# Optimization experiments

Hardware: AMD Instinct MI355X
Metric: run time of the kernel (lower is better)

The kernel has to match this reference:

```python
import jax, jax.numpy as jnp
import numpy as np

N_EMBD = 1024
N_HEAD = 16
STRIDE = 128
C = 8
SEQ = 2048
BATCH = 2


def _sparse_causal_mask(nd, ns, stride, c, dtype):
    # Faithful vectorization of _sparse_attention_mask:
    # column j is globally visible if (j % stride) >= stride - c (the last c
    # columns of each stride block), each query also sees its own stride block,
    # and everything is causally masked (j <= q).
    j = jnp.arange(ns)
    q = jnp.arange(ns)[:, None]
    col_sel = (j % stride) >= (stride - c)          # strided summary columns
    same_block = (j[None, :] // stride) == (q // stride)  # local block
    causal = j[None, :] <= q
    mask = ((col_sel[None, :] | same_block) & causal).astype(dtype)
    return mask[ns - nd:]


def setup_inputs() -> dict:
    key = jax.random.key(0)
    k1, k2, k3 = jax.random.split(key, 3)
    inputs = jax.random.normal(k1, (BATCH, SEQ, N_EMBD), dtype=jnp.float32)
    w_attn = jax.random.normal(k2, (N_EMBD, 3 * N_EMBD), dtype=jnp.float32) * 0.02
    b_attn = jnp.zeros((3 * N_EMBD,), dtype=jnp.float32)
    proj_std = 0.02 / np.sqrt(2 * 24)  # n_layer = 24
    w_proj = jax.random.normal(k3, (N_EMBD, N_EMBD), dtype=jnp.float32) * proj_std
    b_proj = jnp.zeros((N_EMBD,), dtype=jnp.float32)
    return {"inputs": inputs, "w_attn": w_attn, "b_attn": b_attn,
            "w_proj": w_proj, "b_proj": b_proj}


def reference(inputs, w_attn, b_attn, w_proj, b_proj):
    B, S, E = inputs.shape
    H = N_HEAD
    D = E // H
    qkv = inputs @ w_attn + b_attn                     # [B,S,3E]
    q, k, v = jnp.split(qkv, 3, axis=-1)
    def split_heads(x):
        return x.reshape(B, S, H, D).transpose(0, 2, 1, 3)  # [B,H,S,D]
    q, k, v = split_heads(q), split_heads(k), split_heads(v)
    present = jnp.stack([k, v], axis=1)                # [B,2,H,S,D]
    scale = jnp.asarray(D, q.dtype) ** 0.5
    w = jnp.einsum('bhqd,bhkd->bhqk', q, k) / scale    # [B,H,S,S]
    mask = _sparse_causal_mask(S, S, STRIDE, C, w.dtype)
    w = w * mask - 1e10 * (1.0 - mask)
    p = jax.nn.softmax(w, axis=-1).astype(v.dtype)
    h = jnp.einsum('bhqk,bhkd->bhqd', p, v)            # [B,H,S,D]
    h = h.transpose(0, 2, 1, 3).reshape(B, S, E)       # merge heads
    h = h @ w_proj + b_proj
    # dropout p=0.0 (eval) -> identity
    return (h, present)
```

## Files before the change

kernel.cpp:

```cpp
#include <hip/hip_runtime.h>
#include <stdint.h>

typedef unsigned short u16;
typedef unsigned int u32;
typedef __attribute__((ext_vector_type(4))) float f32x4;
typedef __attribute__((ext_vector_type(4))) u16 u16x4;
typedef __attribute__((ext_vector_type(8))) __bf16 bf16x8;

__device__ __forceinline__ u16 f2bf(float f) {
  u32 u = __builtin_bit_cast(u32, f);
  u = (u + 0x7FFFu + ((u >> 16) & 1u)) >> 16;
  return (u16)u;
}

__device__ __forceinline__ void gload_lds16(const void* g, void* l) {
  __builtin_amdgcn_global_load_lds(
      (const __attribute__((address_space(1))) void*)(uintptr_t)(g),
      (__attribute__((address_space(3))) void*)(u32)(uintptr_t)(l),
      16, 0, 0);
}

__global__ __launch_bounds__(256) void k_prep(
    const float* __restrict__ x, u16* __restrict__ xbf,
    const float* __restrict__ wa, u16* __restrict__ wat,
    const float* __restrict__ wp, u16* __restrict__ wpt) {
  __shared__ float tile[32][33];
  const int bid = blockIdx.x, t = threadIdx.x;
  if (bid < 4096) {
    int i = bid * 256 + t;
    f32x4 v = ((const f32x4*)x)[i];
    u16x4 o = { f2bf(v.x), f2bf(v.y), f2bf(v.z), f2bf(v.w) };
    ((u16x4*)xbf)[i] = o;
    return;
  }
  const float* in;
  u16* out;
  int n0, k0, N;
  if (bid < 4096 + 3072) {
    int idx = bid - 4096;
    in = wa; out = wat; N = 3072;
    n0 = (idx % 96) * 32; k0 = (idx / 96) * 32;
  } else {
    int idx = bid - 7168;
    in = wp; out = wpt; N = 1024;
    n0 = (idx & 31) * 32; k0 = (idx >> 5) * 32;
  }
  int c = t & 31, r0 = t >> 5;
#pragma unroll
  for (int i = 0; i < 4; ++i)
    tile[r0 + i * 8][c] = in[(size_t)(k0 + r0 + i * 8) * N + n0 + c];
  __syncthreads();
  int on = t >> 3, ok = (t & 7) * 4;
  u16x4 o = { f2bf(tile[ok + 0][on]), f2bf(tile[ok + 1][on]),
              f2bf(tile[ok + 2][on]), f2bf(tile[ok + 3][on]) };
  *(u16x4*)&out[(size_t)(n0 + on) * 1024 + k0 + ok] = o;
}

__global__ __launch_bounds__(256) void k_kv(const float* __restrict__ present,
                                            u16* __restrict__ kbf,
                                            u16* __restrict__ vtw) {
  __shared__ float tile[32][33];
  const int bid = blockIdx.x, t = threadIdx.x;
  if (bid >= 4096) {
    int i = bid - 4096;
    size_t idx = (size_t)i * 256 + t;
    size_t b = idx >> 19, off = idx & ((1u << 19) - 1);
    f32x4 v = ((const f32x4*)present)[b * (1u << 20) + off];
    u16x4 o = { f2bf(v.x), f2bf(v.y), f2bf(v.z), f2bf(v.w) };
    ((u16x4*)kbf)[idx] = o;
    return;
  }
  int bh = bid >> 7, rem = bid & 127;
  int s0 = (rem >> 1) * 32, d0 = (rem & 1) * 32;
  int b = bh >> 4, h = bh & 15;
  const float* vsrc = present + (((size_t)(b * 2 + 1) * 16 + h) * 2048) * 64;
  u16* vdst = vtw + ((size_t)bh * 64) * 2048;
  int c = t & 31, r0 = t >> 5;
#pragma unroll
  for (int i = 0; i < 4; ++i)
    tile[r0 + i * 8][c] = vsrc[(size_t)(s0 + r0 + i * 8) * 64 + d0 + c];
  __syncthreads();
  int on = t >> 3, ok = (t & 7) * 4;
  u16x4 o = { f2bf(tile[ok + 0][on]), f2bf(tile[ok + 1][on]),
              f2bf(tile[ok + 2][on]), f2bf(tile[ok + 3][on]) };
  *(u16x4*)&vdst[(size_t)(d0 + on) * 2048 + s0 + ok] = o;
}

template <int EPI, int BN>
__global__ __launch_bounds__(256) void k_gemm(
    const u16* __restrict__ A, const u16* __restrict__ Bt,
    const float* __restrict__ bias, u16* __restrict__ outq,
    float* __restrict__ outp, int M, int N, int K) {
  __shared__ u16 a_lds[128 * 64];
  __shared__ u16 b_lds[BN * 64];
  const int t = threadIdx.x;
  const int lane = t & 63, w = t >> 6;

  int m0, n0;
  {
    constexpr int NXT = (EPI == 0) ? 24 : 16;
    constexpr int NCH = (EPI == 0) ? 12 : 8;
    int f = blockIdx.y * NXT + blockIdx.x;
    int xcd = f & 7, idx = f >> 3;
    int mt = (xcd >> 1) * 8 + idx / NCH;
    int nt = (xcd & 1) * NCH + idx % NCH;
    m0 = mt * 128;
    n0 = nt * BN;
  }

  const int srow = t >> 3;
  const int scb = (t & 7) * 16;
  const int ssw = scb ^ ((srow & 7) << 4);
  const size_t pitch = (size_t)K * 2;
  const char* aS = (const char*)A + (size_t)(m0 + srow) * pitch + ssw;
  const char* bS = (const char*)Bt + (size_t)(n0 + srow) * pitch + ssw;
  char* al = (char*)a_lds + t * 16;
  char* bl = (char*)b_lds + t * 16;
  const int wm = (w >> 1) * 64, wn = (w & 1) * (BN / 2);
  const int cc = lane & 15, g = lane >> 4;
  constexpr int NF = BN / 32;

  f32x4 acc[4][NF] = {};

  for (int kt = 0; kt < K; kt += 64) {
    __syncthreads();
#pragma unroll
    for (int i = 0; i < 4; ++i)
      gload_lds16(aS + (size_t)kt * 2 + (size_t)i * 32 * pitch, al + i * 4096);
#pragma unroll
    for (int i = 0; i < BN / 32; ++i)
      gload_lds16(bS + (size_t)kt * 2 + (size_t)i * 32 * pitch, bl + i * 4096);
    __syncthreads();
#pragma unroll
    for (int kk = 0; kk < 2; ++kk) {
      bf16x8 af[4], bf_[NF];
#pragma unroll
      for (int mf = 0; mf < 4; ++mf) {
        int row = wm + mf * 16 + cc;
        af[mf] = *(const bf16x8*)((const char*)a_lds + row * 128 +
                                  ((kk * 64 + g * 16) ^ ((row & 7) << 4)));
      }
#pragma unroll
      for (int nf = 0; nf < NF; ++nf) {
        int row = wn + nf * 16 + cc;
        bf_[nf] = *(const bf16x8*)((const char*)b_lds + row * 128 +
                                   ((kk * 64 + g * 16) ^ ((row & 7) << 4)));
      }
#pragma unroll
      for (int mf = 0; mf < 4; ++mf)
#pragma unroll
        for (int nf = 0; nf < NF; ++nf)
          acc[mf][nf] = __builtin_amdgcn_mfma_f32_16x16x32_bf16(
              af[mf], bf_[nf], acc[mf][nf], 0, 0, 0);
    }
  }

  float bv[NF];
#pragma unroll
  for (int nf = 0; nf < NF; ++nf) bv[nf] = bias[n0 + wn + nf * 16 + cc];

#pragma unroll
  for (int mf = 0; mf < 4; ++mf)
#pragma unroll
    for (int nf = 0; nf < NF; ++nf) {
      int n = n0 + wn + nf * 16 + cc;
      int mb = m0 + wm + mf * 16 + g * 4;
      float v[4];
#pragma unroll
      for (int j = 0; j < 4; ++j) v[j] = acc[mf][nf][j] + bv[nf];
      if (EPI == 1) {
#pragma unroll
        for (int j = 0; j < 4; ++j) outp[(size_t)(mb + j) * N + n] = v[j];
      } else if (n < 1024) {
#pragma unroll
        for (int j = 0; j < 4; ++j) outq[(size_t)(mb + j) * 1024 + n] = f2bf(v[j]);
      } else {
        int n2 = n - 1024;
        int kv = n2 >> 10; n2 &= 1023;
        int hh = n2 >> 6, d = n2 & 63;
        int bb = mb >> 11, ss = mb & 2047;
        float* pr = outp + ((((size_t)bb * 2 + kv) * 16 + hh) * 2048 + ss) * 64 + d;
#pragma unroll
        for (int j = 0; j < 4; ++j) pr[(size_t)j * 64] = v[j];
      }
    }
}

__global__ __launch_bounds__(256) void k_attn(
    const u16* __restrict__ qws, const u16* __restrict__ kbf,
    const u16* __restrict__ vtw, u16* __restrict__ hws) {
  const int qb = blockIdx.x, h = blockIdx.y, b = blockIdx.z;
  const int t = threadIdx.x, lane = t & 63, w = t >> 6;
  const int cc = lane & 15, g = lane >> 4;

  __shared__ u16 k_lds[256 * 64];
  __shared__ u16 p_lds[4][32 * 72];
  __shared__ float rsum[4][32];

  const char* kh = (const char*)kbf + (size_t)(b * 16 + h) * (2048 * 128);
  const char* vh = (const char*)vtw + (size_t)(b * 16 + h) * (64 * 4096);

  {
    int rr = t >> 3, seg = (t & 7) * 16;
#pragma unroll
    for (int i = 0; i < 8; ++i) {
      int r = i * 32 + rr;
      int i2 = r - 128;
      int gr = (r < 128) ? (qb * 128 + r) : ((i2 >> 3) * 128 + 120 + (i2 & 7));
      gload_lds16(kh + (size_t)gr * 128 + (seg ^ ((r & 7) << 4)),
                  (char*)k_lds + i * 4096 + t * 16);
    }
  }

  bf16x8 qf_[2][2];
  {
    const char* qsrc = (const char*)qws +
        (size_t)(b * 2048 + qb * 128 + w * 32 + cc) * 2048 + h * 128 + g * 16;
#pragma unroll
    for (int qf = 0; qf < 2; ++qf)
#pragma unroll
      for (int kk = 0; kk < 2; ++kk)
        qf_[qf][kk] = *(const bf16x8*)(qsrc + (size_t)qf * 16 * 2048 + kk * 64);
  }
  __syncthreads();

  const int nsum = 8 * qb;
  f32x4 o_[2][4] = {};
  float lsum[2] = { 0.f, 0.f };

#pragma unroll 2
  for (int ch = 0; ch < 4; ++ch) {
    f32x4 s[4][2] = {};
#pragma unroll
    for (int kf2 = 0; kf2 < 4; ++kf2) {
      int row = ch * 64 + kf2 * 16 + cc;
      const char* kr = (const char*)k_lds + row * 128;
#pragma unroll
      for (int kk = 0; kk < 2; ++kk) {
        bf16x8 kfr = *(const bf16x8*)(kr + ((kk * 64 + g * 16) ^ ((cc & 7) << 4)));
#pragma unroll
        for (int qf = 0; qf < 2; ++qf)
          s[kf2][qf] = __builtin_amdgcn_mfma_f32_16x16x32_bf16(
              kfr, qf_[qf][kk], s[kf2][qf], 0, 0, 0);
      }
    }
#pragma unroll
    for (int qf = 0; qf < 2; ++qf) {
      int q_local = w * 32 + qf * 16 + cc;
#pragma unroll
      for (int kf2 = 0; kf2 < 4; ++kf2) {
#pragma unroll
        for (int j = 0; j < 4; ++j) {
          int key = ch * 64 + kf2 * 16 + g * 4 + j;
          bool vis = (key < 128) ? (key <= q_local) : (key - 128 < nsum);
          float p = vis ? exp2f(s[kf2][qf][j] * 0.180336884f) : 0.f;
          s[kf2][qf][j] = p;
          lsum[qf] += p;
        }
        u16x4 pw = { f2bf(s[kf2][qf][0]), f2bf(s[kf2][qf][1]),
                     f2bf(s[kf2][qf][2]), f2bf(s[kf2][qf][3]) };
        *(u16x4*)&p_lds[w][(qf * 16 + cc) * 72 + kf2 * 16 + g * 4] = pw;
      }
    }
#pragma unroll
    for (int kk = 0; kk < 2; ++kk) {
      bf16x8 pa[2], vb[4];
#pragma unroll
      for (int mf = 0; mf < 2; ++mf)
        pa[mf] = *(const bf16x8*)((const char*)p_lds[w] +
                                  (mf * 16 + cc) * 144 + kk * 64 + g * 16);
      int cb = (ch < 2) ? (qb * 256 + ch * 128 + kk * 64 + g * 16)
                        : (((ch - 2) * 8 + kk * 4 + g) * 256 + 240);
#pragma unroll
      for (int nf = 0; nf < 4; ++nf)
        vb[nf] = *(const bf16x8*)(vh + (size_t)(nf * 16 + cc) * 4096 + cb);
#pragma unroll
      for (int mf = 0; mf < 2; ++mf)
#pragma unroll
        for (int nf = 0; nf < 4; ++nf)
          o_[mf][nf] = __builtin_amdgcn_mfma_f32_16x16x32_bf16(pa[mf], vb[nf],
                                                               o_[mf][nf], 0, 0, 0);
    }
  }

#pragma unroll
  for (int qf = 0; qf < 2; ++qf) {
    float sum = lsum[qf];
    sum += __shfl_xor(sum, 16);
    sum += __shfl_xor(sum, 32);
    if (g == 0) rsum[w][qf * 16 + cc] = sum;
  }
#pragma unroll
  for (int mf = 0; mf < 2; ++mf)
#pragma unroll
    for (int j = 0; j < 4; ++j) {
      float inv = 1.0f / rsum[w][mf * 16 + g * 4 + j];
      size_t row = (size_t)(b * 2048 + qb * 128 + w * 32 + mf * 16 + g * 4 + j);
#pragma unroll
      for (int nf = 0; nf < 4; ++nf)
        hws[row * 1024 + h * 64 + nf * 16 + cc] = f2bf(o_[mf][nf][j] * inv);
    }
}

extern "C" void kernel_launch(void* const* d_in, const int* in_sizes, int n_in,
                              void* d_out, int out_size, void* d_ws, size_t ws_size,
                              hipStream_t stream) {
  const float* x      = (const float*)d_in[0];
  const float* w_attn = (const float*)d_in[1];
  const float* b_attn = (const float*)d_in[2];
  const float* w_proj = (const float*)d_in[3];
  const float* b_proj = (const float*)d_in[4];
  float* h_out   = (float*)d_out;
  float* present = (float*)d_out + 4194304;

  char* ws = (char*)d_ws;
  u16* xbf = (u16*)(ws);
  u16* qws = (u16*)(ws + (8u << 20));
  u16* wat = (u16*)(ws + (16u << 20));
  u16* wpt = (u16*)(ws + (22u << 20));
  u16* kbf = (u16*)(ws + (24u << 20));
  u16* vtw = (u16*)(ws + (32u << 20));
  u16* hws = xbf;

  k_prep<<<8192, 256, 0, stream>>>(x, xbf, w_attn, wat, w_proj, wpt);
  k_gemm<0, 128><<<dim3(24, 32), 256, 0, stream>>>(xbf, wat, b_attn, qws,
                                                   present, 4096, 3072, 1024);
  k_kv<<<8192, 256, 0, stream>>>(present, kbf, vtw);
  k_attn<<<dim3(16, 16, 2), 256, 0, stream>>>(qws, kbf, vtw, hws);
  k_gemm<1, 64><<<dim3(16, 32), 256, 0, stream>>>(hws, wpt, b_proj, nullptr,
                                                  h_out, 4096, 1024, 1024);
}
```

Baseline: 90.77 us.

## Stage GEMM epilogue through LDS for vector stores and fuse K bf16 conversion

The GEMM epilogue now writes each wave's accumulator tile into shared memory and reads it back row-major, so global stores become 16-byte (or 8-byte bf16) vectorized row writes instead of scattered 4-byte column writes. The QKV GEMM also emits the bf16 copy of K directly, which removes the K-conversion half of the k_kv kernel and its re-read of present. The cost is an extra LDS round trip and a barrier in the epilogue.

```diff
diff --git a/kernel.cpp b/kernel.cpp
--- a/kernel.cpp
+++ b/kernel.cpp
@@ -57,19 +57,9 @@
 }
 
 __global__ __launch_bounds__(256) void k_kv(const float* __restrict__ present,
-                                            u16* __restrict__ kbf,
                                             u16* __restrict__ vtw) {
   __shared__ float tile[32][33];
   const int bid = blockIdx.x, t = threadIdx.x;
-  if (bid >= 4096) {
-    int i = bid - 4096;
-    size_t idx = (size_t)i * 256 + t;
-    size_t b = idx >> 19, off = idx & ((1u << 19) - 1);
-    f32x4 v = ((const f32x4*)present)[b * (1u << 20) + off];
-    u16x4 o = { f2bf(v.x), f2bf(v.y), f2bf(v.z), f2bf(v.w) };
-    ((u16x4*)kbf)[idx] = o;
-    return;
-  }
   int bh = bid >> 7, rem = bid & 127;
   int s0 = (rem >> 1) * 32, d0 = (rem & 1) * 32;
   int b = bh >> 4, h = bh & 15;
@@ -90,9 +80,10 @@
 __global__ __launch_bounds__(256) void k_gemm(
     const u16* __restrict__ A, const u16* __restrict__ Bt,
     const float* __restrict__ bias, u16* __restrict__ outq,
-    float* __restrict__ outp, int M, int N, int K) {
-  __shared__ u16 a_lds[128 * 64];
-  __shared__ u16 b_lds[BN * 64];
+    float* __restrict__ outp, u16* __restrict__ kbf, int M, int N, int K) {
+  __shared__ u16 lds_all[128 * 64 + BN * 64];
+  u16* a_lds = lds_all;
+  u16* b_lds = lds_all + 128 * 64;
   const int t = threadIdx.x;
   const int lane = t & 63, w = t >> 6;
 
@@ -159,31 +150,46 @@
 #pragma unroll
   for (int nf = 0; nf < NF; ++nf) bv[nf] = bias[n0 + wn + nf * 16 + cc];
 
-#pragma unroll
-  for (int mf = 0; mf < 4; ++mf)
-#pragma unroll
-    for (int nf = 0; nf < NF; ++nf) {
-      int n = n0 + wn + nf * 16 + cc;
-      int mb = m0 + wm + mf * 16 + g * 4;
-      float v[4];
-#pragma unroll
-      for (int j = 0; j < 4; ++j) v[j] = acc[mf][nf][j] + bv[nf];
+  __syncthreads();
+  constexpr int CW = (EPI == 0) ? 64 : 32;
+  constexpr int SST = CW + 4;
+  constexpr int REPS = (16 * (CW / 4)) / 64;
+  float* scw = (float*)lds_all + w * 16 * SST;
+  const int rrow = lane & 15;
+  const int qbase = lane >> 4;
+
+#pragma unroll
+  for (int mf = 0; mf < 4; ++mf) {
+#pragma unroll
+    for (int nf = 0; nf < NF; ++nf)
+#pragma unroll
+      for (int j = 0; j < 4; ++j)
+        scw[(g * 4 + j) * SST + nf * 16 + cc] = acc[mf][nf][j] + bv[nf];
+    int m_row = m0 + wm + mf * 16 + rrow;
+#pragma unroll
+    for (int rep = 0; rep < REPS; ++rep) {
+      int quad = qbase + rep * 4;
+      f32x4 v = *(f32x4*)&scw[rrow * SST + quad * 4];
+      int nc = n0 + wn + quad * 4;
       if (EPI == 1) {
-#pragma unroll
-        for (int j = 0; j < 4; ++j) outp[(size_t)(mb + j) * N + n] = v[j];
-      } else if (n < 1024) {
-#pragma unroll
-        for (int j = 0; j < 4; ++j) outq[(size_t)(mb + j) * 1024 + n] = f2bf(v[j]);
+        *(f32x4*)&outp[(size_t)m_row * N + nc] = v;
+      } else if (nc < 1024) {
+        u16x4 o = { f2bf(v.x), f2bf(v.y), f2bf(v.z), f2bf(v.w) };
+        *(u16x4*)&outq[(size_t)m_row * 1024 + nc] = o;
       } else {
-        int n2 = n - 1024;
+        int n2 = nc - 1024;
         int kv = n2 >> 10; n2 &= 1023;
         int hh = n2 >> 6, d = n2 & 63;
-        int bb = mb >> 11, ss = mb & 2047;
-        float* pr = outp + ((((size_t)bb * 2 + kv) * 16 + hh) * 2048 + ss) * 64 + d;
-#pragma unroll
-        for (int j = 0; j < 4; ++j) pr[(size_t)j * 64] = v[j];
-      }
-    }
+        int bb = m_row >> 11, ss = m_row & 2047;
+        *(f32x4*)(outp + ((((size_t)bb * 2 + kv) * 16 + hh) * 2048 + ss) * 64 +
+                  d) = v;
+        if (kv == 0) {
+          u16x4 o = { f2bf(v.x), f2bf(v.y), f2bf(v.z), f2bf(v.w) };
+          *(u16x4*)&kbf[(((size_t)bb * 16 + hh) * 2048 + ss) * 64 + d] = o;
+        }
+      }
+    }
+  }
 }
 
 __global__ __launch_bounds__(256) void k_attn(
@@ -324,9 +330,9 @@
 
   k_prep<<<8192, 256, 0, stream>>>(x, xbf, w_attn, wat, w_proj, wpt);
   k_gemm<0, 128><<<dim3(24, 32), 256, 0, stream>>>(xbf, wat, b_attn, qws,
-                                                   present, 4096, 3072, 1024);
-  k_kv<<<8192, 256, 0, stream>>>(present, kbf, vtw);
+                                                   present, kbf, 4096, 3072, 1024);
+  k_kv<<<4096, 256, 0, stream>>>(present, vtw);
   k_attn<<<dim3(16, 16, 2), 256, 0, stream>>>(qws, kbf, vtw, hws);
   k_gemm<1, 64><<<dim3(16, 32), 256, 0, stream>>>(hws, wpt, b_proj, nullptr,
-                                                  h_out, 4096, 1024, 1024);
-}
+                                                  h_out, nullptr, 4096, 1024, 1024);
+}
```

Result: no change. 92.48 us (+1.9%).

## Double-buffer GEMM LDS tiles to overlap global loads with MFMA compute

Applied to the files above, without the earlier changes.

The GEMM kernel now keeps two LDS buffers and issues the direct-to-LDS global loads for the next K tile before computing on the current one. Manual vmcnt waits and barriers replace the two syncthreads per iteration, and MFMA sections are bracketed by setprio so math waves get issue priority. It doubles LDS usage, which may lower occupancy, and hardcodes K=1024 (16 iterations) along with fixed vmcnt counts tied to the load count per stage.

```diff
diff --git a/kernel.cpp b/kernel.cpp
--- a/kernel.cpp
+++ b/kernel.cpp
@@ -87,12 +87,12 @@
 }
 
 template <int EPI, int BN>
-__global__ __launch_bounds__(256) void k_gemm(
+__global__ __launch_bounds__(256) void k_gemm2(
     const u16* __restrict__ A, const u16* __restrict__ Bt,
     const float* __restrict__ bias, u16* __restrict__ outq,
     float* __restrict__ outp, int M, int N, int K) {
-  __shared__ u16 a_lds[128 * 64];
-  __shared__ u16 b_lds[BN * 64];
+  __shared__ u16 a_lds[2][128 * 64];
+  __shared__ u16 b_lds[2][BN * 64];
   const int t = threadIdx.x;
   const int lane = t & 63, w = t >> 6;
 
@@ -114,45 +114,63 @@
   const size_t pitch = (size_t)K * 2;
   const char* aS = (const char*)A + (size_t)(m0 + srow) * pitch + ssw;
   const char* bS = (const char*)Bt + (size_t)(n0 + srow) * pitch + ssw;
-  char* al = (char*)a_lds + t * 16;
-  char* bl = (char*)b_lds + t * 16;
   const int wm = (w >> 1) * 64, wn = (w & 1) * (BN / 2);
   const int cc = lane & 15, g = lane >> 4;
   constexpr int NF = BN / 32;
 
+  auto stage = [&](int bi, int tj) {
+#pragma unroll
+    for (int i = 0; i < 4; ++i)
+      gload_lds16(aS + (size_t)tj * 128 + (size_t)i * 32 * pitch,
+                  (char*)a_lds[bi] + i * 4096 + t * 16);
+#pragma unroll
+    for (int i = 0; i < BN / 32; ++i)
+      gload_lds16(bS + (size_t)tj * 128 + (size_t)i * 32 * pitch,
+                  (char*)b_lds[bi] + i * 4096 + t * 16);
+  };
+
   f32x4 acc[4][NF] = {};
 
-  for (int kt = 0; kt < K; kt += 64) {
-    __syncthreads();
-#pragma unroll
-    for (int i = 0; i < 4; ++i)
-      gload_lds16(aS + (size_t)kt * 2 + (size_t)i * 32 * pitch, al + i * 4096);
-#pragma unroll
-    for (int i = 0; i < BN / 32; ++i)
-      gload_lds16(bS + (size_t)kt * 2 + (size_t)i * 32 * pitch, bl + i * 4096);
-    __syncthreads();
+  stage(0, 0);
+  for (int j = 0; j < 16; ++j) {
+    const int bi = j & 1, nx = bi ^ 1;
+    if (j < 15) {
+      stage(nx, j + 1);
+      if constexpr (BN == 128)
+        asm volatile("s_waitcnt vmcnt(8)\n\ts_barrier" ::: "memory");
+      else
+        asm volatile("s_waitcnt vmcnt(6)\n\ts_barrier" ::: "memory");
+    } else {
+      asm volatile("s_waitcnt vmcnt(0)\n\ts_barrier" ::: "memory");
+    }
+
 #pragma unroll
     for (int kk = 0; kk < 2; ++kk) {
       bf16x8 af[4], bf_[NF];
 #pragma unroll
       for (int mf = 0; mf < 4; ++mf) {
         int row = wm + mf * 16 + cc;
-        af[mf] = *(const bf16x8*)((const char*)a_lds + row * 128 +
+        af[mf] = *(const bf16x8*)((const char*)a_lds[bi] + row * 128 +
                                   ((kk * 64 + g * 16) ^ ((row & 7) << 4)));
       }
 #pragma unroll
       for (int nf = 0; nf < NF; ++nf) {
         int row = wn + nf * 16 + cc;
-        bf_[nf] = *(const bf16x8*)((const char*)b_lds + row * 128 +
+        bf_[nf] = *(const bf16x8*)((const char*)b_lds[bi] + row * 128 +
                                    ((kk * 64 + g * 16) ^ ((row & 7) << 4)));
       }
+      __builtin_amdgcn_s_setprio(1);
 #pragma unroll
       for (int mf = 0; mf < 4; ++mf)
 #pragma unroll
         for (int nf = 0; nf < NF; ++nf)
           acc[mf][nf] = __builtin_amdgcn_mfma_f32_16x16x32_bf16(
               af[mf], bf_[nf], acc[mf][nf], 0, 0, 0);
-    }
+      __builtin_amdgcn_s_setprio(0);
+    }
+
+    if (j < 15)
+      asm volatile("s_waitcnt lgkmcnt(0)\n\ts_barrier" ::: "memory");
   }
 
   float bv[NF];
@@ -323,10 +341,10 @@
   u16* hws = xbf;
 
   k_prep<<<8192, 256, 0, stream>>>(x, xbf, w_attn, wat, w_proj, wpt);
-  k_gemm<0, 128><<<dim3(24, 32), 256, 0, stream>>>(xbf, wat, b_attn, qws,
-                                                   present, 4096, 3072, 1024);
+  k_gemm2<0, 128><<<dim3(24, 32), 256, 0, stream>>>(xbf, wat, b_attn, qws,
+                                                    present, 4096, 3072, 1024);
   k_kv<<<8192, 256, 0, stream>>>(present, kbf, vtw);
   k_attn<<<dim3(16, 16, 2), 256, 0, stream>>>(qws, kbf, vtw, hws);
-  k_gemm<1, 64><<<dim3(16, 32), 256, 0, stream>>>(hws, wpt, b_proj, nullptr,
-                                                  h_out, 4096, 1024, 1024);
-}
+  k_gemm2<1, 64><<<dim3(16, 32), 256, 0, stream>>>(hws, wpt, b_proj, nullptr,
+                                                   h_out, 4096, 1024, 1024);
+}
```

New measurement: 88.91 us. 1.02x faster.
